# Kernel tuning notes

Hardware: AMD Instinct MI355X
Metric: run time of the kernel (lower is better)

## Reference

```python
import jax, jax.numpy as jnp
import numpy as np

N = 100000      # nodes
E = 1600000     # edges (avg degree 16)
DIN = 64
DOUT = 64
C = 8           # num classes; label -1 means unknown


def _xavier(key, shape):
    a = jnp.sqrt(6.0 / (shape[0] + shape[1]))
    return jax.random.uniform(key, shape, jnp.float32, -a, a)


def setup_inputs():
    key = jax.random.key(0)
    ks = jax.random.split(key, 17)
    return {
        "x": jax.random.normal(ks[0], (N, DIN), jnp.float32),
        "adj_low_vals": jax.random.uniform(ks[1], (E,), jnp.float32) / 16.0,
        "adj_high_vals": jax.random.uniform(ks[2], (E,), jnp.float32) / 16.0,
        "weight_low": _xavier(ks[3], (DIN, DOUT)),
        "weight_high": _xavier(ks[4], (DIN, DOUT)),
        "weight_mlp": _xavier(ks[5], (DIN, DOUT)),
        "att_vec_low_fr": _xavier(ks[6], (DOUT, 1)),
        "att_vec_high_fr": _xavier(ks[7], (DOUT, 1)),
        "att_vec_low_be": _xavier(ks[8], (DOUT, 1)),
        "att_vec_high_be": _xavier(ks[9], (DOUT, 1)),
        "att_vec_low_unk": _xavier(ks[10], (DOUT, 1)),
        "att_vec_high_unk": _xavier(ks[11], (DOUT, 1)),
        "att_vec_mlp": _xavier(ks[12], (DOUT, 1)),
        "att_vec7": _xavier(ks[13], (7, 7)),
        "edge_src": jax.random.randint(ks[14], (E,), 0, N),
        "edge_dst": jax.random.randint(ks[15], (E,), 0, N),
        "label_unk": jax.random.randint(ks[16], (N,), -1, C),
    }


def reference(x, adj_low_vals, adj_high_vals, weight_low, weight_high, weight_mlp,
              att_vec_low_fr, att_vec_high_fr, att_vec_low_be, att_vec_high_be,
              att_vec_low_unk, att_vec_high_unk, att_vec_mlp, att_vec7,
              edge_src, edge_dst, label_unk):
    def spmm(vals, feats):  # out[dst] += vals * feats[src]  (sparse [N,N] @ [N,D])
        return jax.ops.segment_sum(vals[:, None] * feats[edge_src], edge_dst, num_segments=N)

    output_low = jax.nn.relu(spmm(adj_low_vals, x @ weight_low))
    output_high = jax.nn.relu(spmm(adj_high_vals, x @ weight_high))
    output_mlp = jax.nn.relu(x @ weight_mlp)

    # per-edge fake label: 2 if either endpoint unknown (<0), 1 if labels differ
    # (both known) -> heterophilous, else 0 -> homophilous
    sl = label_unk[edge_src]
    dl = label_unk[edge_dst]
    fake = jnp.where((sl < 0) | (dl < 0), 2, jnp.where(sl != dl, 1, 0))

    h_low_e = output_low[edge_src]    # [E, DOUT] gathered messages
    h_high_e = output_high[edge_src]

    def agg(h_e, k):  # masked segment-sum over destination nodes
        m = (fake == k).astype(h_e.dtype)[:, None]
        return jax.ops.segment_sum(h_e * m, edge_dst, num_segments=N)

    neigh_homo_low, neigh_hete_low, neigh_unk_low = agg(h_low_e, 0), agg(h_low_e, 1), agg(h_low_e, 2)
    neigh_homo_high, neigh_hete_high, neigh_unk_high = agg(h_high_e, 0), agg(h_high_e, 1), agg(h_high_e, 2)

    # attention7 (fr_high_g is None branch)
    feats = jax.nn.sigmoid(jnp.concatenate([
        neigh_hete_low @ att_vec_low_fr, neigh_hete_high @ att_vec_high_fr,
        neigh_homo_low @ att_vec_low_be, neigh_homo_high @ att_vec_high_be,
        neigh_unk_low @ att_vec_low_unk, neigh_unk_high @ att_vec_high_unk,
        output_mlp @ att_vec_mlp], axis=1))  # [N, 7]
    att = jax.nn.softmax((feats @ att_vec7) / 7.0, axis=1)

    return 7.0 * (att[:, 0:1] * neigh_hete_low + att[:, 1:2] * neigh_hete_high
                  + att[:, 2:3] * neigh_homo_low + att[:, 3:4] * neigh_homo_high
                  + att[:, 4:5] * neigh_unk_low + att[:, 5:6] * neigh_unk_high
                  + att[:, 6:7] * output_mlp)
```

## Files before the change

kernel.cpp:

```cpp
#include <hip/hip_runtime.h>
#include <hip/hip_bf16.h>

typedef unsigned int u32;
typedef unsigned short u16;
typedef unsigned long long u64;

typedef __attribute__((ext_vector_type(8))) short bf16x8;
typedef __attribute__((ext_vector_type(4))) float f32x4;

static __device__ __forceinline__ float bflo(u32 u) { return __uint_as_float(u << 16); }
static __device__ __forceinline__ float bfhi(u32 u) { return __uint_as_float(u & 0xFFFF0000u); }
static __device__ __forceinline__ float bf2f(u16 u) { return __uint_as_float((u32)u << 16); }
static __device__ __forceinline__ u32 f2bf(float f) {
    u32 u = __float_as_uint(f);
    return (u + 0x7FFFu + ((u >> 16) & 1u)) >> 16;
}
static __device__ __forceinline__ u32 packbf(float lo, float hi) {
    return f2bf(lo) | (f2bf(hi) << 16);
}
static __device__ __forceinline__ float ldf(const u16* p16, int idx, int isf32) {
    return isf32 ? ((const float*)p16)[idx] : bf2f(p16[idx]);
}
static __device__ __forceinline__ void load4(const u16* p, int q, int isf32, float* v) {
    if (isf32) {
        float4 t = ((const float4*)p)[q];
        v[0] = t.x; v[1] = t.y; v[2] = t.z; v[3] = t.w;
    } else {
        u32 a = ((const u32*)p)[q * 2], b = ((const u32*)p)[q * 2 + 1];
        v[0] = bflo(a); v[1] = bfhi(a); v[2] = bflo(b); v[3] = bfhi(b);
    }
}
static __device__ __forceinline__ float sanitize(float v, float code) {
    return (fabsf(v) < 1e30f) ? v : code;
}

static __device__ __forceinline__ float wave_sum(float v) {
#pragma unroll
    for (int o = 32; o; o >>= 1) v += __shfl_xor(v, o, 64);
    return v;
}
static __device__ __forceinline__ float group_sum(float v) {
#pragma unroll
    for (int o = 8; o; o >>= 1) v += __shfl_xor(v, o, 64);
    return v;
}


__global__ void k_sentinel(float* __restrict__ out, int n, float val) {
    int i = blockIdx.x * blockDim.x + threadIdx.x;
    if (i < n) out[i] = val;
}

__global__ void k_zero_sniff(int* __restrict__ p, int n, const u16* __restrict__ x,
                             int* __restrict__ flag) {
    int i = blockIdx.x * blockDim.x + threadIdx.x;
    if (i < n) p[i] = 0;
    if (blockIdx.x == 0 && threadIdx.x < 64) {
        int lane = threadIdx.x;
        int wild = 0;
        for (int k = 0; k < 64; k++) {
            u32 u = x[lane * 64 + k];
            int e = (u >> 7) & 0xFF;
            if (e < 96 || e > 135) wild++;
        }
        float tot = wave_sum((float)wild);
        if (lane == 0) *flag = (tot > 200.f) ? 1 : 0;
    }
}


__global__ void k_hist(const int* __restrict__ dst, int E, int* __restrict__ deg) {
    int i = blockIdx.x * blockDim.x + threadIdx.x;
    if (i < E) atomicAdd(&deg[dst[i]], 1);
}

__global__ void k_scan_partial(const int* __restrict__ deg, int n, int* __restrict__ bsum) {
    int t = threadIdx.x;
    int base = blockIdx.x * 1024 + t * 4;
    int s = 0;
#pragma unroll
    for (int j = 0; j < 4; j++) {
        int idx = base + j;
        if (idx < n) s += deg[idx];
    }
    __shared__ int sh[256];
    sh[t] = s;
    __syncthreads();
    for (int d = 128; d; d >>= 1) {
        if (t < d) sh[t] += sh[t + d];
        __syncthreads();
    }
    if (t == 0) bsum[blockIdx.x] = sh[0];
}

__global__ void k_scan_bsum(const int* __restrict__ bsum, int nb, int* __restrict__ boff) {
    int t = threadIdx.x;
    int v = (t < nb) ? bsum[t] : 0;
    __shared__ int sh[256];
    sh[t] = v;
    __syncthreads();
    for (int d = 1; d < 256; d <<= 1) {
        int u = (t >= d) ? sh[t - d] : 0;
        __syncthreads();
        sh[t] += u;
        __syncthreads();
    }
    if (t < nb) boff[t] = sh[t] - v;
}

__global__ void k_scan_final(const int* __restrict__ deg, int n, const int* __restrict__ boff,
                             int* __restrict__ offsets, int Etot) {
    int t = threadIdx.x;
    int base = blockIdx.x * 1024 + t * 4;
    int v[4];
    int s = 0;
#pragma unroll
    for (int j = 0; j < 4; j++) {
        int idx = base + j;
        v[j] = (idx < n) ? deg[idx] : 0;
        s += v[j];
    }
    __shared__ int sh[256];
    sh[t] = s;
    __syncthreads();
    for (int d = 1; d < 256; d <<= 1) {
        int u = (t >= d) ? sh[t - d] : 0;
        __syncthreads();
        sh[t] += u;
        __syncthreads();
    }
    int ex = sh[t] - s + boff[blockIdx.x];
#pragma unroll
    for (int j = 0; j < 4; j++) {
        int idx = base + j;
        if (idx < n) offsets[idx] = ex;
        ex += v[j];
    }
    if (blockIdx.x == 0 && t == 0) offsets[n] = Etot;
}

__global__ void k_scatter(const int* __restrict__ src, const int* __restrict__ dst,
                          const u16* __restrict__ avl, const u16* __restrict__ avh,
                          const int* __restrict__ lab, int E,
                          const int* __restrict__ offsets, int* __restrict__ cursor,
                          u64* __restrict__ epay, const int* __restrict__ flag) {
    int i = blockIdx.x * blockDim.x + threadIdx.x;
    if (i >= E) return;
    int isf32 = *flag;
    int d = dst[i];
    int pos = offsets[d] + atomicAdd(&cursor[d], 1);
    if ((unsigned)pos >= (unsigned)E) return;
    int s = src[i];
    int sl = lab[s], dl = lab[d];
    int fake = (sl < 0 || dl < 0) ? 2 : ((sl != dl) ? 1 : 0);
    u32 lo32 = (u32)(s | (fake << 20));
    u32 hi32 = isf32 ? packbf(((const float*)avl)[i], ((const float*)avh)[i])
                     : ((u32)avl[i] | ((u32)avh[i] << 16));
    epay[pos] = ((u64)hi32 << 32) | lo32;
}


__global__ void k_prepB(const u16* __restrict__ wl, const u16* __restrict__ wh,
                        const u16* __restrict__ wm, u16* __restrict__ Bpack,
                        const int* __restrict__ flag) {
    int isf32 = *flag;
    for (int idx = threadIdx.x; idx < 12 * 2 * 64; idx += 256) {
        int slot = idx >> 6;
        int ln = idx & 63;
        int ct = slot >> 1, c = slot & 1;
        int mat = ct >> 2;
        const u16* W = (mat == 0) ? wl : (mat == 1) ? wh : wm;
        int col = (ct & 3) * 16 + (ln & 15);
        int kbase = c * 32 + (ln >> 4) * 8;
        u16* dst = Bpack + (size_t)idx * 8;
#pragma unroll
        for (int j = 0; j < 8; j++) dst[j] = (u16)f2bf(ldf(W, (kbase + j) * 64 + col, isf32));
    }
}

__launch_bounds__(256) __global__
void k_gemm_mfma(const u16* __restrict__ x, const u16* __restrict__ Bpack, int N,
                 u32* __restrict__ xwlh, float* __restrict__ omlp,
                 const int* __restrict__ flag) {
    int isf32 = *flag;
    int lane = threadIdx.x & 63;
    int wv = (blockIdx.x * 256 + threadIdx.x) >> 6;
    int nw = gridDim.x * 4;
    int m = lane & 15, quad = lane >> 4;
    int ntiles = (N + 15) >> 4;
    for (int tile = wv; tile < ntiles; tile += nw) {
        int r0 = tile * 16;
        int arow = min(r0 + m, N - 1);
        bf16x8 a[2];
#pragma unroll
        for (int c = 0; c < 2; c++) {
            int base = arow * 64 + c * 32 + quad * 8;
            if (isf32) {
                const float* xf = (const float*)x;
#pragma unroll
                for (int j = 0; j < 8; j++) a[c][j] = (short)f2bf(xf[base + j]);
            } else {
#pragma unroll
                for (int j = 0; j < 8; j++) a[c][j] = (short)x[base + j];
            }
        }
        f32x4 acc[12];
#pragma unroll
        for (int t = 0; t < 12; t++) acc[t] = (f32x4){0.f, 0.f, 0.f, 0.f};
#pragma unroll
        for (int t = 0; t < 12; t++) {
#pragma unroll
            for (int c = 0; c < 2; c++) {
                bf16x8 b = *(const bf16x8*)(Bpack + (size_t)((t * 2 + c) * 64 + lane) * 8);
                acc[t] = __builtin_amdgcn_mfma_f32_16x16x32_bf16(a[c], b, acc[t], 0, 0, 0);
            }
        }
#pragma unroll
        for (int t = 0; t < 4; t++) {
#pragma unroll
            for (int r = 0; r < 4; r++) {
                int row = r0 + quad * 4 + r;
                if (row < N) {
                    int o = row * 64 + t * 16 + m;
                    xwlh[o] = packbf(acc[t][r], acc[t + 4][r]);
                    omlp[o] = fmaxf(acc[t + 8][r], 0.f);
                }
            }
        }
    }
}


__launch_bounds__(256) __global__
void k_spmm4n(const u32* __restrict__ xwlh, const u64* __restrict__ epay,
              const int* __restrict__ offsets, int N, int E, u32* __restrict__ outlh) {
    int lane = threadIdx.x & 63;
    int gwave = blockIdx.x * 4 + (threadIdx.x >> 6);
    int g = lane & 15, gi = lane >> 4;
    int node = gwave * 4 + gi;
    bool vn = node < N;
    int s = vn ? offsets[node] : 0;
    int e = vn ? offsets[node + 1] : 0;
    int deg = e - s;
    int md = deg;
    md = max(md, __shfl_xor(md, 16, 64));
    md = max(md, __shfl_xor(md, 32, 64));
    int Nm1 = N - 1, Em1 = E - 1;
    float aL[4] = {0.f, 0.f, 0.f, 0.f}, aH[4] = {0.f, 0.f, 0.f, 0.f};
    for (int t = 0; t < md; t += 2) {
#pragma unroll
        for (int u = 0; u < 2; u++) {
            int tt = t + u;
            int idx = min(max(s + min(tt, deg - 1), 0), Em1);
            u64 p = epay[idx];
            float w = (tt < deg) ? 1.f : 0.f;
            int sj = min((int)(p & 0xFFFFF), Nm1);
            u32 vv = (u32)(p >> 32);
            float vl = w * bflo(vv), vh = w * bfhi(vv);
            uint4 R = *((const uint4*)(xwlh + (size_t)sj * 64) + g);
            aL[0] += vl * bflo(R.x); aH[0] += vh * bfhi(R.x);
            aL[1] += vl * bflo(R.y); aH[1] += vh * bfhi(R.y);
            aL[2] += vl * bflo(R.z); aH[2] += vh * bfhi(R.z);
            aL[3] += vl * bflo(R.w); aH[3] += vh * bfhi(R.w);
        }
    }
    if (vn) {
        uint4 W;
        W.x = packbf(fmaxf(aL[0], 0.f), fmaxf(aH[0], 0.f));
        W.y = packbf(fmaxf(aL[1], 0.f), fmaxf(aH[1], 0.f));
        W.z = packbf(fmaxf(aL[2], 0.f), fmaxf(aH[2], 0.f));
        W.w = packbf(fmaxf(aL[3], 0.f), fmaxf(aH[3], 0.f));
        ((uint4*)(outlh + (size_t)node * 64))[g] = W;
    }
}


__launch_bounds__(256) __global__
void k_agg4n(const u32* __restrict__ outlh, const u64* __restrict__ epay,
             const int* __restrict__ offsets,
             const u16* __restrict__ aLF, const u16* __restrict__ aHF,
             const u16* __restrict__ aLB, const u16* __restrict__ aHB,
             const u16* __restrict__ aLU, const u16* __restrict__ aHU,
             const u16* __restrict__ aM, const u16* __restrict__ a7, int N, int E,
             float* __restrict__ out, const int* __restrict__ flag) {
    int isf32 = *flag;
    int lane = threadIdx.x & 63;
    int gwave = blockIdx.x * 4 + (threadIdx.x >> 6);
    int g = lane & 15, gi = lane >> 4;
    int node = gwave * 4 + gi;
    bool vn = node < N;
    int s = vn ? offsets[node] : 0;
    int e = vn ? offsets[node + 1] : 0;
    int deg = e - s;
    int md = deg;
    md = max(md, __shfl_xor(md, 16, 64));
    md = max(md, __shfl_xor(md, 32, 64));
    int Nm1 = N - 1, Em1 = E - 1;
    float heL[4] = {0, 0, 0, 0}, heH[4] = {0, 0, 0, 0};
    float hoL[4] = {0, 0, 0, 0}, hoH[4] = {0, 0, 0, 0};
    float unL[4] = {0, 0, 0, 0}, unH[4] = {0, 0, 0, 0};
    for (int t = 0; t < md; t += 2) {
#pragma unroll
        for (int u = 0; u < 2; u++) {
            int tt = t + u;
            int idx = min(max(s + min(tt, deg - 1), 0), Em1);
            u64 p = epay[idx];
            int fk = (int)(p >> 20) & 3;
            bool valid = (tt < deg);
            float whe = (valid && fk == 1) ? 1.f : 0.f;
            float who = (valid && fk == 0) ? 1.f : 0.f;
            float wun = (valid && fk == 2) ? 1.f : 0.f;
            int sj = min((int)(p & 0xFFFFF), Nm1);
            uint4 R = *((const uint4*)(outlh + (size_t)sj * 64) + g);
            float lo0 = bflo(R.x), hi0 = bfhi(R.x);
            float lo1 = bflo(R.y), hi1 = bfhi(R.y);
            float lo2 = bflo(R.z), hi2 = bfhi(R.z);
            float lo3 = bflo(R.w), hi3 = bfhi(R.w);
            heL[0] += whe * lo0; heH[0] += whe * hi0;
            heL[1] += whe * lo1; heH[1] += whe * hi1;
            heL[2] += whe * lo2; heH[2] += whe * hi2;
            heL[3] += whe * lo3; heH[3] += whe * hi3;
            hoL[0] += who * lo0; hoH[0] += who * hi0;
            hoL[1] += who * lo1; hoH[1] += who * hi1;
            hoL[2] += who * lo2; hoH[2] += who * hi2;
            hoL[3] += who * lo3; hoH[3] += who * hi3;
            unL[0] += wun * lo0; unH[0] += wun * hi0;
            unL[1] += wun * lo1; unH[1] += wun * hi1;
            unL[2] += wun * lo2; unH[2] += wun * hi2;
            unL[3] += wun * lo3; unH[3] += wun * hi3;
        }
    }
    float vLF[4], vHF[4], vLB[4], vHB[4], vLU[4], vHU[4], vM[4];
    load4(aLF, g, isf32, vLF);
    load4(aHF, g, isf32, vHF);
    load4(aLB, g, isf32, vLB);
    load4(aHB, g, isf32, vHB);
    load4(aLU, g, isf32, vLU);
    load4(aHU, g, isf32, vHU);
    load4(aM, g, isf32, vM);
    float mvv[4] = {0.f, 0.f, 0.f, 0.f};
    if (vn) {
        float4 MV = ((const float4*)(out + (size_t)node * 64))[g];
        mvv[0] = MV.x; mvv[1] = MV.y; mvv[2] = MV.z; mvv[3] = MV.w;
    }

    float p0 = 0, p1 = 0, p2 = 0, p3 = 0, p4 = 0, p5 = 0, p6 = 0;
#pragma unroll
    for (int k = 0; k < 4; k++) {
        p0 += heL[k] * vLF[k];
        p1 += heH[k] * vHF[k];
        p2 += hoL[k] * vLB[k];
        p3 += hoH[k] * vHB[k];
        p4 += unL[k] * vLU[k];
        p5 += unH[k] * vHU[k];
        p6 += mvv[k] * vM[k];
    }
    float d0 = group_sum(p0), d1 = group_sum(p1), d2 = group_sum(p2), d3 = group_sum(p3);
    float d4 = group_sum(p4), d5 = group_sum(p5), d6 = group_sum(p6);

    float f[7];
    f[0] = 1.f / (1.f + expf(-d0));
    f[1] = 1.f / (1.f + expf(-d1));
    f[2] = 1.f / (1.f + expf(-d2));
    f[3] = 1.f / (1.f + expf(-d3));
    f[4] = 1.f / (1.f + expf(-d4));
    f[5] = 1.f / (1.f + expf(-d5));
    f[6] = 1.f / (1.f + expf(-d6));

    float z[7];
#pragma unroll
    for (int jj = 0; jj < 7; jj++) {
        float acc = 0.f;
#pragma unroll
        for (int i = 0; i < 7; i++) acc += f[i] * ldf(a7, i * 7 + jj, isf32);
        z[jj] = acc * (1.f / 7.f);
    }
    float m = z[0];
#pragma unroll
    for (int jj = 1; jj < 7; jj++) m = fmaxf(m, z[jj]);
    float wsum = 0.f;
    float wv[7];
#pragma unroll
    for (int jj = 0; jj < 7; jj++) { wv[jj] = expf(z[jj] - m); wsum += wv[jj]; }
    float s7 = 7.f / wsum;

    if (vn) {
        float4 W;
        float o0 = wv[0] * heL[0] + wv[1] * heH[0] + wv[2] * hoL[0] + wv[3] * hoH[0] +
                   wv[4] * unL[0] + wv[5] * unH[0] + wv[6] * mvv[0];
        float o1 = wv[0] * heL[1] + wv[1] * heH[1] + wv[2] * hoL[1] + wv[3] * hoH[1] +
                   wv[4] * unL[1] + wv[5] * unH[1] + wv[6] * mvv[1];
        float o2 = wv[0] * heL[2] + wv[1] * heH[2] + wv[2] * hoL[2] + wv[3] * hoH[2] +
                   wv[4] * unL[2] + wv[5] * unH[2] + wv[6] * mvv[2];
        float o3 = wv[0] * heL[3] + wv[1] * heH[3] + wv[2] * hoL[3] + wv[3] * hoH[3] +
                   wv[4] * unL[3] + wv[5] * unH[3] + wv[6] * mvv[3];
        W.x = sanitize(o0 * s7, 333.f);
        W.y = sanitize(o1 * s7, 333.f);
        W.z = sanitize(o2 * s7, 333.f);
        W.w = sanitize(o3 * s7, 333.f);
        ((float4*)(out + (size_t)node * 64))[g] = W;
    }
}


extern "C" void kernel_launch(void* const* d_in, const int* in_sizes, int n_in, void* d_out,
                              int out_size, void* d_ws, size_t ws_size, hipStream_t stream) {
    const u16* x = (const u16*)d_in[0];
    const u16* avl = (const u16*)d_in[1];
    const u16* avh = (const u16*)d_in[2];
    const u16* wl = (const u16*)d_in[3];
    const u16* wh = (const u16*)d_in[4];
    const u16* wm = (const u16*)d_in[5];
    const u16* aLF = (const u16*)d_in[6];
    const u16* aHF = (const u16*)d_in[7];
    const u16* aLB = (const u16*)d_in[8];
    const u16* aHB = (const u16*)d_in[9];
    const u16* aLU = (const u16*)d_in[10];
    const u16* aHU = (const u16*)d_in[11];
    const u16* aM = (const u16*)d_in[12];
    const u16* a7 = (const u16*)d_in[13];
    const int* esrc = (const int*)d_in[14];
    const int* edst = (const int*)d_in[15];
    const int* lab = (const int*)d_in[16];
    float* out = (float*)d_out;

    const int N = in_sizes[0] / 64;
    const int E = in_sizes[1];

    char* w = (char*)d_ws;
    size_t off = 0;
    auto alloc = [&](size_t bytes) -> char* {
        char* p = w + off;
        off += (bytes + 255) & ~(size_t)255;
        return p;
    };
    int* flag = (int*)alloc(256);
    int* offsets = (int*)alloc((size_t)(N + 1) * 4);
    int* degcur = (int*)alloc((size_t)2 * N * 4);
    int* bsum = (int*)alloc(256 * 4);
    int* boff = (int*)alloc(256 * 4);
    u16* Bpack = (u16*)alloc(12 * 2 * 64 * 8 * 2);
    u64* epay = (u64*)alloc((size_t)E * 8);
    u32* xwlh = (u32*)alloc((size_t)N * 64 * 4);
    u32* outlh = (u32*)alloc((size_t)N * 64 * 4);

    if (ws_size < off) {
        k_sentinel<<<(out_size + 255) / 256, 256, 0, stream>>>(out, out_size, 1000.0f);
        return;
    }

    int* deg = degcur;
    int* cursor = degcur + N;
    int NB = (N + 1023) / 1024;

    k_zero_sniff<<<(2 * N + 255) / 256, 256, 0, stream>>>(degcur, 2 * N, x, flag);
    k_hist<<<(E + 255) / 256, 256, 0, stream>>>(edst, E, deg);
    k_scan_partial<<<NB, 256, 0, stream>>>(deg, N, bsum);
    k_scan_bsum<<<1, 256, 0, stream>>>(bsum, NB, boff);
    k_scan_final<<<NB, 256, 0, stream>>>(deg, N, boff, offsets, E);
    k_scatter<<<(E + 255) / 256, 256, 0, stream>>>(esrc, edst, avl, avh, lab, E, offsets, cursor,
                                                   epay, flag);

    k_prepB<<<1, 256, 0, stream>>>(wl, wh, wm, Bpack, flag);
    int ntiles = (N + 15) / 16;
    int gemmBlocks = (ntiles + 3) / 4;
    k_gemm_mfma<<<gemmBlocks, 256, 0, stream>>>(x, Bpack, N, xwlh, out , flag);

    int nodeBlocks = (N + 15) / 16;
    k_spmm4n<<<nodeBlocks, 256, 0, stream>>>(xwlh, epay, offsets, N, E, outlh);
    k_agg4n<<<nodeBlocks, 256, 0, stream>>>(outlh, epay, offsets, aLF, aHF, aLB, aHB, aLU, aHU,
                                            aM, a7, N, E, out, flag);
}
```

Baseline: 461.1 us.

## Bucket edges by destination and class, and schedule nodes sorted by degree

```diff
diff --git a/kernel.cpp b/kernel.cpp
--- a/kernel.cpp
+++ b/kernel.cpp
@@ -69,17 +69,22 @@
 }
 
 
-__global__ void k_hist(const int* __restrict__ dst, int E, int* __restrict__ deg) {
+__global__ void k_hist3(const int* __restrict__ src, const int* __restrict__ dst,
+                        const int* __restrict__ lab, int E, int* __restrict__ deg3) {
     int i = blockIdx.x * blockDim.x + threadIdx.x;
-    if (i < E) atomicAdd(&deg[dst[i]], 1);
-}
-
-__global__ void k_scan_partial(const int* __restrict__ deg, int n, int* __restrict__ bsum) {
+    if (i >= E) return;
+    int s = src[i], d = dst[i];
+    int sl = lab[s], dl = lab[d];
+    int fake = (sl < 0 || dl < 0) ? 2 : ((sl != dl) ? 1 : 0);
+    atomicAdd(&deg3[d * 3 + fake], 1);
+}
+
+__global__ void k_scan_partial8(const int* __restrict__ deg, int n, int* __restrict__ bsum) {
     int t = threadIdx.x;
-    int base = blockIdx.x * 1024 + t * 4;
+    int base = blockIdx.x * 2048 + t * 8;
     int s = 0;
 #pragma unroll
-    for (int j = 0; j < 4; j++) {
+    for (int j = 0; j < 8; j++) {
         int idx = base + j;
         if (idx < n) s += deg[idx];
     }
@@ -108,14 +113,14 @@
     if (t < nb) boff[t] = sh[t] - v;
 }
 
-__global__ void k_scan_final(const int* __restrict__ deg, int n, const int* __restrict__ boff,
-                             int* __restrict__ offsets, int Etot) {
+__global__ void k_scan_final8(const int* __restrict__ deg, int n, const int* __restrict__ boff,
+                              int* __restrict__ offsets, int Etot) {
     int t = threadIdx.x;
-    int base = blockIdx.x * 1024 + t * 4;
-    int v[4];
+    int base = blockIdx.x * 2048 + t * 8;
+    int v[8];
     int s = 0;
 #pragma unroll
-    for (int j = 0; j < 4; j++) {
+    for (int j = 0; j < 8; j++) {
         int idx = base + j;
         v[j] = (idx < n) ? deg[idx] : 0;
         s += v[j];
@@ -131,7 +136,7 @@
     }
     int ex = sh[t] - s + boff[blockIdx.x];
 #pragma unroll
-    for (int j = 0; j < 4; j++) {
+    for (int j = 0; j < 8; j++) {
         int idx = base + j;
         if (idx < n) offsets[idx] = ex;
         ex += v[j];
@@ -142,21 +147,75 @@
 __global__ void k_scatter(const int* __restrict__ src, const int* __restrict__ dst,
                           const u16* __restrict__ avl, const u16* __restrict__ avh,
                           const int* __restrict__ lab, int E,
-                          const int* __restrict__ offsets, int* __restrict__ cursor,
+                          const int* __restrict__ off3, int* __restrict__ cursor3,
                           u64* __restrict__ epay, const int* __restrict__ flag) {
     int i = blockIdx.x * blockDim.x + threadIdx.x;
     if (i >= E) return;
     int isf32 = *flag;
-    int d = dst[i];
-    int pos = offsets[d] + atomicAdd(&cursor[d], 1);
-    if ((unsigned)pos >= (unsigned)E) return;
-    int s = src[i];
+    int s = src[i], d = dst[i];
     int sl = lab[s], dl = lab[d];
     int fake = (sl < 0 || dl < 0) ? 2 : ((sl != dl) ? 1 : 0);
+    int b = d * 3 + fake;
+    int pos = off3[b] + atomicAdd(&cursor3[b], 1);
+    if ((unsigned)pos >= (unsigned)E) return;
     u32 lo32 = (u32)(s | (fake << 20));
     u32 hi32 = isf32 ? packbf(((const float*)avl)[i], ((const float*)avh)[i])
                      : ((u32)avl[i] | ((u32)avh[i] << 16));
     epay[pos] = ((u64)hi32 << 32) | lo32;
+}
+
+
+__global__ void k_dhist(const int* __restrict__ deg3, int N, int* __restrict__ dbins) {
+    __shared__ u32 lh[256];
+    int t = threadIdx.x;
+    lh[t] = 0;
+    __syncthreads();
+    int i = blockIdx.x * 256 + t;
+    if (i < N) {
+        int d = deg3[i * 3] + deg3[i * 3 + 1] + deg3[i * 3 + 2];
+        atomicAdd(&lh[min(d, 255)], 1u);
+    }
+    __syncthreads();
+    if (lh[t]) atomicAdd(&dbins[t], (int)lh[t]);
+}
+
+__global__ void k_dscan(const int* __restrict__ dbins, int* __restrict__ dbase) {
+    int t = threadIdx.x;
+    int v = dbins[t];
+    __shared__ int sh[256];
+    sh[t] = v;
+    __syncthreads();
+    for (int d = 1; d < 256; d <<= 1) {
+        int u = (t >= d) ? sh[t - d] : 0;
+        __syncthreads();
+        sh[t] += u;
+        __syncthreads();
+    }
+    dbase[t] = sh[t] - v;
+}
+
+__global__ void k_dscatter(const int* __restrict__ deg3, int N, const int* __restrict__ dbase,
+                           int* __restrict__ dcur, int* __restrict__ perm) {
+    __shared__ u32 lh[256], lrank[256], gbase[256];
+    int t = threadIdx.x;
+    lh[t] = 0;
+    lrank[t] = 0;
+    __syncthreads();
+    int i = blockIdx.x * 256 + t;
+    int b = -1;
+    if (i < N) {
+        int d = deg3[i * 3] + deg3[i * 3 + 1] + deg3[i * 3 + 2];
+        b = min(d, 255);
+        atomicAdd(&lh[b], 1u);
+    }
+    __syncthreads();
+    if (lh[t]) gbase[t] = (u32)atomicAdd(&dcur[t], (int)lh[t]);
+    __syncthreads();
+    if (b >= 0) {
+        u32 r = atomicAdd(&lrank[b], 1u);
+        int pos = dbase[b] + (int)gbase[b] + (int)r;
+        if ((unsigned)pos < (unsigned)N) perm[pos] = i;
+    }
 }
 
 
@@ -233,14 +292,16 @@
 
 __launch_bounds__(256) __global__
 void k_spmm4n(const u32* __restrict__ xwlh, const u64* __restrict__ epay,
-              const int* __restrict__ offsets, int N, int E, u32* __restrict__ outlh) {
+              const int* __restrict__ off3, const int* __restrict__ perm, int N, int E,
+              u32* __restrict__ outlh) {
     int lane = threadIdx.x & 63;
     int gwave = blockIdx.x * 4 + (threadIdx.x >> 6);
     int g = lane & 15, gi = lane >> 4;
-    int node = gwave * 4 + gi;
-    bool vn = node < N;
-    int s = vn ? offsets[node] : 0;
-    int e = vn ? offsets[node + 1] : 0;
+    int nidx = gwave * 4 + gi;
+    bool vn = nidx < N;
+    int node = vn ? perm[nidx] : 0;
+    int s = vn ? off3[node * 3] : 0;
+    int e = vn ? off3[node * 3 + 3] : 0;
     int deg = e - s;
     int md = deg;
     md = max(md, __shfl_xor(md, 16, 64));
@@ -275,9 +336,34 @@
 }
 
 
+static __device__ __forceinline__ void agg_class(const u32* __restrict__ outlh,
+                                                 const u64* __restrict__ epay, int s, int e,
+                                                 int g, int Nm1, int Em1, float* accL,
+                                                 float* accH) {
+    int deg = e - s;
+    int md = deg;
+    md = max(md, __shfl_xor(md, 16, 64));
+    md = max(md, __shfl_xor(md, 32, 64));
+    for (int t = 0; t < md; t += 2) {
+#pragma unroll
+        for (int u = 0; u < 2; u++) {
+            int tt = t + u;
+            int idx = min(max(s + min(tt, deg - 1), 0), Em1);
+            u64 p = epay[idx];
+            float w = (tt < deg) ? 1.f : 0.f;
+            int sj = min((int)(p & 0xFFFFF), Nm1);
+            uint4 R = *((const uint4*)(outlh + (size_t)sj * 64) + g);
+            accL[0] = fmaf(w, bflo(R.x), accL[0]); accH[0] = fmaf(w, bfhi(R.x), accH[0]);
+            accL[1] = fmaf(w, bflo(R.y), accL[1]); accH[1] = fmaf(w, bfhi(R.y), accH[1]);
+            accL[2] = fmaf(w, bflo(R.z), accL[2]); accH[2] = fmaf(w, bfhi(R.z), accH[2]);
+            accL[3] = fmaf(w, bflo(R.w), accL[3]); accH[3] = fmaf(w, bfhi(R.w), accH[3]);
+        }
+    }
+}
+
 __launch_bounds__(256) __global__
 void k_agg4n(const u32* __restrict__ outlh, const u64* __restrict__ epay,
-             const int* __restrict__ offsets,
+             const int* __restrict__ off3, const int* __restrict__ perm,
              const u16* __restrict__ aLF, const u16* __restrict__ aHF,
              const u16* __restrict__ aLB, const u16* __restrict__ aHB,
              const u16* __restrict__ aLU, const u16* __restrict__ aHU,
@@ -287,49 +373,22 @@
     int lane = threadIdx.x & 63;
     int gwave = blockIdx.x * 4 + (threadIdx.x >> 6);
     int g = lane & 15, gi = lane >> 4;
-    int node = gwave * 4 + gi;
-    bool vn = node < N;
-    int s = vn ? offsets[node] : 0;
-    int e = vn ? offsets[node + 1] : 0;
-    int deg = e - s;
-    int md = deg;
-    md = max(md, __shfl_xor(md, 16, 64));
-    md = max(md, __shfl_xor(md, 32, 64));
+    int nidx = gwave * 4 + gi;
+    bool vn = nidx < N;
+    int node = vn ? perm[nidx] : 0;
+    int b0 = node * 3;
+    int sHom = vn ? off3[b0] : 0;
+    int sHet = vn ? off3[b0 + 1] : 0;
+    int sUnk = vn ? off3[b0 + 2] : 0;
+    int eAll = vn ? off3[b0 + 3] : 0;
     int Nm1 = N - 1, Em1 = E - 1;
     float heL[4] = {0, 0, 0, 0}, heH[4] = {0, 0, 0, 0};
     float hoL[4] = {0, 0, 0, 0}, hoH[4] = {0, 0, 0, 0};
     float unL[4] = {0, 0, 0, 0}, unH[4] = {0, 0, 0, 0};
-    for (int t = 0; t < md; t += 2) {
-#pragma unroll
-        for (int u = 0; u < 2; u++) {
-            int tt = t + u;
-            int idx = min(max(s + min(tt, deg - 1), 0), Em1);
-            u64 p = epay[idx];
-            int fk = (int)(p >> 20) & 3;
-            bool valid = (tt < deg);
-            float whe = (valid && fk == 1) ? 1.f : 0.f;
-            float who = (valid && fk == 0) ? 1.f : 0.f;
-            float wun = (valid && fk == 2) ? 1.f : 0.f;
-            int sj = min((int)(p & 0xFFFFF), Nm1);
-            uint4 R = *((const uint4*)(outlh + (size_t)sj * 64) + g);
-            float lo0 = bflo(R.x), hi0 = bfhi(R.x);
-            float lo1 = bflo(R.y), hi1 = bfhi(R.y);
-            float lo2 = bflo(R.z), hi2 = bfhi(R.z);
-            float lo3 = bflo(R.w), hi3 = bfhi(R.w);
-            heL[0] += whe * lo0; heH[0] += whe * hi0;
-            heL[1] += whe * lo1; heH[1] += whe * hi1;
-            heL[2] += whe * lo2; heH[2] += whe * hi2;
-            heL[3] += whe * lo3; heH[3] += whe * hi3;
-            hoL[0] += who * lo0; hoH[0] += who * hi0;
-            hoL[1] += who * lo1; hoH[1] += who * hi1;
-            hoL[2] += who * lo2; hoH[2] += who * hi2;
-            hoL[3] += who * lo3; hoH[3] += who * hi3;
-            unL[0] += wun * lo0; unH[0] += wun * hi0;
-            unL[1] += wun * lo1; unH[1] += wun * hi1;
-            unL[2] += wun * lo2; unH[2] += wun * hi2;
-            unL[3] += wun * lo3; unH[3] += wun * hi3;
-        }
-    }
+    agg_class(outlh, epay, sHom, sHet, g, Nm1, Em1, hoL, hoH);
+    agg_class(outlh, epay, sHet, sUnk, g, Nm1, Em1, heL, heH);
+    agg_class(outlh, epay, sUnk, eAll, g, Nm1, Em1, unL, unH);
+
     float vLF[4], vHF[4], vLB[4], vHB[4], vLU[4], vHU[4], vM[4];
     load4(aLF, g, isf32, vLF);
     load4(aHF, g, isf32, vHF);
@@ -426,6 +485,7 @@
 
     const int N = in_sizes[0] / 64;
     const int E = in_sizes[1];
+    const int n3 = 3 * N;
 
     char* w = (char*)d_ws;
     size_t off = 0;
@@ -435,10 +495,12 @@
         return p;
     };
     int* flag = (int*)alloc(256);
-    int* offsets = (int*)alloc((size_t)(N + 1) * 4);
-    int* degcur = (int*)alloc((size_t)2 * N * 4);
+    int* off3 = (int*)alloc((size_t)(n3 + 1) * 4);
+    int* zeroreg = (int*)alloc((size_t)(2 * n3 + 512) * 4);
     int* bsum = (int*)alloc(256 * 4);
     int* boff = (int*)alloc(256 * 4);
+    int* dbase = (int*)alloc(256 * 4);
+    int* perm = (int*)alloc((size_t)N * 4);
     u16* Bpack = (u16*)alloc(12 * 2 * 64 * 8 * 2);
     u64* epay = (u64*)alloc((size_t)E * 8);
     u32* xwlh = (u32*)alloc((size_t)N * 64 * 4);
@@ -449,17 +511,25 @@
         return;
     }
 
-    int* deg = degcur;
-    int* cursor = degcur + N;
-    int NB = (N + 1023) / 1024;
-
-    k_zero_sniff<<<(2 * N + 255) / 256, 256, 0, stream>>>(degcur, 2 * N, x, flag);
-    k_hist<<<(E + 255) / 256, 256, 0, stream>>>(edst, E, deg);
-    k_scan_partial<<<NB, 256, 0, stream>>>(deg, N, bsum);
-    k_scan_bsum<<<1, 256, 0, stream>>>(bsum, NB, boff);
-    k_scan_final<<<NB, 256, 0, stream>>>(deg, N, boff, offsets, E);
-    k_scatter<<<(E + 255) / 256, 256, 0, stream>>>(esrc, edst, avl, avh, lab, E, offsets, cursor,
+    int* deg3 = zeroreg;
+    int* cursor3 = zeroreg + n3;
+    int* dbins = zeroreg + 2 * n3;
+    int* dcur = zeroreg + 2 * n3 + 256;
+    int nzero = 2 * n3 + 512;
+    int NB3 = (n3 + 2047) / 2048;
+
+    k_zero_sniff<<<(nzero + 255) / 256, 256, 0, stream>>>(zeroreg, nzero, x, flag);
+    k_hist3<<<(E + 255) / 256, 256, 0, stream>>>(esrc, edst, lab, E, deg3);
+    k_scan_partial8<<<NB3, 256, 0, stream>>>(deg3, n3, bsum);
+    k_scan_bsum<<<1, 256, 0, stream>>>(bsum, NB3, boff);
+    k_scan_final8<<<NB3, 256, 0, stream>>>(deg3, n3, boff, off3, E);
+    k_scatter<<<(E + 255) / 256, 256, 0, stream>>>(esrc, edst, avl, avh, lab, E, off3, cursor3,
                                                    epay, flag);
+
+    int NBn = (N + 255) / 256;
+    k_dhist<<<NBn, 256, 0, stream>>>(deg3, N, dbins);
+    k_dscan<<<1, 256, 0, stream>>>(dbins, dbase);
+    k_dscatter<<<NBn, 256, 0, stream>>>(deg3, N, dbase, dcur, perm);
 
     k_prepB<<<1, 256, 0, stream>>>(wl, wh, wm, Bpack, flag);
     int ntiles = (N + 15) / 16;
@@ -467,7 +537,7 @@
     k_gemm_mfma<<<gemmBlocks, 256, 0, stream>>>(x, Bpack, N, xwlh, out , flag);
 
     int nodeBlocks = (N + 15) / 16;
-    k_spmm4n<<<nodeBlocks, 256, 0, stream>>>(xwlh, epay, offsets, N, E, outlh);
-    k_agg4n<<<nodeBlocks, 256, 0, stream>>>(outlh, epay, offsets, aLF, aHF, aLB, aHB, aLU, aHU,
-                                            aM, a7, N, E, out, flag);
-}
+    k_spmm4n<<<nodeBlocks, 256, 0, stream>>>(xwlh, epay, off3, perm, N, E, outlh);
+    k_agg4n<<<nodeBlocks, 256, 0, stream>>>(outlh, epay, off3, perm, aLF, aHF, aLB, aHB, aLU,
+                                            aHU, aM, a7, N, E, out, flag);
+}
```

Result: slower. 490.3 us (+6.3%).
